# Optimization experiments

Hardware: AMD Instinct MI355X
Metric: run time of the kernel (lower is better)

The kernel has to match this reference:

```python
import jax, jax.numpy as jnp
import numpy as np
from jax import lax

INPUT_SIZE = 512
THRESHOLD = 0.5
IOU_TH = 0.3
MAX_ROIS = 32   # py_cpu_nms(...)[:32]
ROI = 7
NEG = jnp.float32(-1e30)


def _make_anchors(fh, fw, stride):
    # 3 scales x 3 ratios = 9 anchors per cell, laid out in (h, w, anchor)
    # order to match permute(0,2,3,1).view(-1) of the conv heads.
    scales = np.array([32.0, 64.0, 128.0])
    ratios = np.array([0.5, 1.0, 2.0])
    ws = (scales[:, None] * np.sqrt(ratios)[None, :]).reshape(-1)
    hs = (scales[:, None] / np.sqrt(ratios)[None, :]).reshape(-1)
    cy = (np.arange(fh) + 0.5) * stride
    cx = (np.arange(fw) + 0.5) * stride
    CX, CY = np.meshgrid(cx, cy)
    CX = CX[..., None]; CY = CY[..., None]
    a = np.stack([CX - ws / 2, CY - hs / 2, CX + ws / 2, CY + hs / 2], axis=-1)
    return jnp.asarray(a.reshape(-1, 4), jnp.float32)


def setup_inputs() -> dict:
    key = jax.random.key(0)
    k1, k2, k3 = jax.random.split(key, 3)
    B, C, FH, FW, A, stride = 4, 256, 64, 64, 9, 8
    featureMap = jax.random.normal(k1, (B, C, FH, FW), jnp.float32)
    # small init so sigmoid scores spread across threshold and exp(tw) stays sane
    w_cls = jax.random.normal(k2, (A, C, 3, 3), jnp.float32) * 0.05
    w_loc = jax.random.normal(k3, (4 * A, C, 3, 3), jnp.float32) * 0.01
    prior_anchor = _make_anchors(FH, FW, stride)
    return {"featureMap": featureMap, "prior_anchor": prior_anchor,
            "w_cls": w_cls, "w_loc": w_loc, "stride": stride}


def _conv(x, w):
    return lax.conv_general_dilated(x, w, (1, 1), "SAME",
                                    dimension_numbers=("NCHW", "OIHW", "NCHW"))


def _decode(loc, anchors):
    aw = anchors[:, 2] - anchors[:, 0]
    ah = anchors[:, 3] - anchors[:, 1]
    acx = anchors[:, 0] + 0.5 * aw
    acy = anchors[:, 1] + 0.5 * ah
    cx = acx + loc[:, 0] * aw
    cy = acy + loc[:, 1] * ah
    w = aw * jnp.exp(loc[:, 2])
    h = ah * jnp.exp(loc[:, 3])
    return jnp.stack([cx - 0.5 * w, cy - 0.5 * h, cx + 0.5 * w, cy + 0.5 * h], axis=1)


def _iou_one(box, boxes):
    xx1 = jnp.maximum(box[0], boxes[:, 0]); yy1 = jnp.maximum(box[1], boxes[:, 1])
    xx2 = jnp.minimum(box[2], boxes[:, 2]); yy2 = jnp.minimum(box[3], boxes[:, 3])
    inter = jnp.clip(xx2 - xx1, 0) * jnp.clip(yy2 - yy1, 0)
    a1 = (box[2] - box[0]) * (box[3] - box[1])
    a2 = (boxes[:, 2] - boxes[:, 0]) * (boxes[:, 3] - boxes[:, 1])
    return inter / (a1 + a2 - inter + 1e-9)


def _nms(boxes, scores, valid):
    # greedy NMS, fixed MAX_ROIS rounds (== sort-by-score py_cpu_nms + [:32])
    N = scores.shape[0]
    s0 = jnp.where(valid, scores, -1.0)

    def body(i, carry):
        s, picks, ok = carry
        idx = jnp.argmax(s)
        good = s[idx] > 0.0
        picks = picks.at[i].set(idx.astype(jnp.int32))
        ok = ok.at[i].set(good)
        sup = (_iou_one(boxes[idx], boxes) > IOU_TH) | (jnp.arange(N) == idx)
        return (jnp.where(sup, -1.0, s), picks, ok)

    _, picks, ok = lax.fori_loop(
        0, MAX_ROIS, body,
        (s0, jnp.zeros(MAX_ROIS, jnp.int32), jnp.zeros(MAX_ROIS, bool)))
    return picks, ok


def _ceil_div(a, b):
    return -(-a // b)


def _adaptive_maxpool(feat, box):
    # feat: [C, FH, FW]; box: int32 [x1, y1, x2, y2] in feature-map coords.
    # Faithful F.adaptive_max_pool2d bins: start=floor(i*h/7), end=ceil((i+1)*h/7).
    FH, FW = feat.shape[1], feat.shape[2]
    x1, y1, x2, y2 = box[0], box[1], box[2], box[3]
    h = y2 - y1; w = x2 - x1
    i = jnp.arange(ROI)
    rs = y1 + (i * h) // ROI; re = y1 + _ceil_div((i + 1) * h, ROI)
    cs = x1 + (i * w) // ROI; ce = x1 + _ceil_div((i + 1) * w, ROI)
    hh = jnp.arange(FH); ww = jnp.arange(FW)
    rm = jnp.where((hh >= rs[:, None]) & (hh < re[:, None]), 0.0, NEG)  # [7, FH]
    cm = jnp.where((ww >= cs[:, None]) & (ww < ce[:, None]), 0.0, NEG)  # [7, FW]
    t = jnp.max(feat[None] + rm[:, None, :, None], axis=2)              # [7, C, FW]
    out = jnp.max(t[:, None] + cm[None, :, None, :], axis=3)            # [7, 7, C]
    return jnp.transpose(out, (2, 0, 1))                                # [C, 7, 7]


def reference(featureMap, prior_anchor, w_cls, w_loc, stride):
    B, C, FH, FW = featureMap.shape
    cls = jax.nn.sigmoid(_conv(featureMap, w_cls))                      # [B, A, FH, FW]
    cls = jnp.transpose(cls, (0, 2, 3, 1)).reshape(B, -1)               # [B, N]
    loc = jnp.transpose(_conv(featureMap, w_loc), (0, 2, 3, 1)).reshape(B, -1, 4)
    boxes = jax.vmap(_decode, in_axes=(0, None))(loc, prior_anchor)     # [B, N, 4]
    boxes = jnp.clip(boxes, 0.0, float(INPUT_SIZE))                     # clamp(0, input_size)
    valid = (cls > THRESHOLD) \
          & (boxes[..., 2] - boxes[..., 0] >= 2 * stride) \
          & (boxes[..., 3] - boxes[..., 1] >= 2 * stride)
    picks, ok = jax.vmap(_nms)(boxes, cls, valid)                       # [B, 32]
    sel_boxes = jnp.take_along_axis(boxes, picks[..., None], axis=1)    # [B, 32, 4]
    sel_scores = jnp.take_along_axis(cls, picks, axis=1)                # [B, 32]
    eval_boxes = jnp.where(
        ok[..., None],
        jnp.concatenate([sel_boxes, sel_scores[..., None]], axis=-1), 0.0)
    # src_coordinate.int() / stride -> integer feature-map coords
    ib = sel_boxes.astype(jnp.int32) // stride
    fx1 = jnp.clip(ib[..., 0], 0, FW - 1); fy1 = jnp.clip(ib[..., 1], 0, FH - 1)
    fx2 = jnp.clip(ib[..., 2], fx1 + 1, FW); fy2 = jnp.clip(ib[..., 3], fy1 + 1, FH)
    fb = jnp.stack([fx1, fy1, fx2, fy2], axis=-1).reshape(-1, 4)        # [B*32, 4]
    img = jnp.repeat(jnp.arange(B), MAX_ROIS)
    rois = lax.map(lambda a: _adaptive_maxpool(featureMap[a[1]], a[0]), (fb, img))
    rois = jnp.where(ok.reshape(-1)[:, None, None, None], rois, 0.0)    # [B*32, 256, 7, 7]
    return eval_boxes, ok, rois
```

## Files before the change

kernel.cpp:

```cpp
#include <hip/hip_runtime.h>
#include <hip/hip_bf16.h>

#define FHH 64
#define FWW 64
#define CIN 256
#define NB 4
#define NA 9
#define NANCH 36864
#define NPOS 4096
#define OC_TOTAL 45
#define OCP 48
#define MAXROIS 32
#define ROI 7
#define NEGV -1e30f
#define NCHUNK 576
#define NTH 16

typedef unsigned long long u64;

__global__ __launch_bounds__(256) void wtrans_kernel(
    const float* __restrict__ wcls,
    const float* __restrict__ wloc,
    float* __restrict__ wT,
    int* __restrict__ gcnt)
{
    if (blockIdx.x == 0 && threadIdx.x < NB * NTH) gcnt[threadIdx.x] = 0;
    int idx = blockIdx.x * 256 + threadIdx.x;
    int o = idx % 48;
    int rest = idx / 48;
    int tap = rest % 9;
    int c = rest / 9;
    float v = 0.f;
    if (o < OC_TOTAL) {
        v = (o < NA) ? wcls[((size_t)o * CIN + c) * 9 + tap]
                     : wloc[((size_t)(o - NA) * CIN + c) * 9 + tap];
    }
    wT[idx] = v;
}

__global__ __launch_bounds__(256) void conv_kernel(
    const float* __restrict__ feat,
    const float* __restrict__ wT,
    float* __restrict__ partial,
    int nkg, int cpk)
{
    __shared__ float flds[16][18][20];

    int blk = blockIdx.x;
    int low = blk & 7;
    int rest = blk >> 3;
    int kg = rest % nkg;
    int uhi = rest / nkg;
    int unit = uhi * 8 + low;
    int b = unit >> 4;
    int tile = unit & 15;

    int ty0 = (tile >> 2) * 16;
    int tx0 = (tile & 3) * 16;

    int pb = threadIdx.x & 63;
    int q = __builtin_amdgcn_readfirstlane(threadIdx.x >> 6);
    int ry0 = (pb >> 3) * 2;
    int rx0 = (pb & 7) * 2;

    int cbase = kg * cpk;

    float acc[2][2][12];
#pragma unroll
    for (int py = 0; py < 2; ++py)
#pragma unroll
        for (int px = 0; px < 2; ++px)
#pragma unroll
            for (int o = 0; o < 12; ++o) acc[py][px][o] = 0.f;

    for (int c0 = 0; c0 < cpk; c0 += 16) {
        __syncthreads();
        for (int idx = threadIdx.x; idx < 16 * 324; idx += 256) {
            int c = idx / 324;
            int r = idx - c * 324;
            int y = r / 18;
            int x = r - y * 18;
            int gy = ty0 + y - 1;
            int gx = tx0 + x - 1;
            float v = 0.f;
            if ((unsigned)gy < FHH && (unsigned)gx < FWW)
                v = feat[((size_t)(b * CIN + cbase + c0 + c) * FHH + gy) * FWW + gx];
            flds[c][y][x] = v;
        }
        __syncthreads();

        const float* wq = wT + (size_t)(cbase + c0) * 432 + q * 12;
        for (int c = 0; c < 16; ++c) {
            float f[4][4];
#pragma unroll
            for (int r = 0; r < 4; ++r) {
                float2 a0 = *(const float2*)&flds[c][ry0 + r][rx0];
                float2 a1 = *(const float2*)&flds[c][ry0 + r][rx0 + 2];
                f[r][0] = a0.x; f[r][1] = a0.y; f[r][2] = a1.x; f[r][3] = a1.y;
            }
#pragma unroll
            for (int tap = 0; tap < 9; ++tap) {
                int dy = tap / 3, dx = tap % 3;
                const float* wp = wq + (c * 9 + tap) * 48;
                float w[12];
#pragma unroll
                for (int o = 0; o < 12; ++o) w[o] = wp[o];
#pragma unroll
                for (int py = 0; py < 2; ++py)
#pragma unroll
                for (int px = 0; px < 2; ++px) {
                    float fv = f[py + dy][px + dx];
#pragma unroll
                    for (int o = 0; o < 12; ++o)
                        acc[py][px][o] += fv * w[o];
                }
            }
        }
    }

    float* pout = partial + ((size_t)kg * NB + b) * OCP * NPOS;
#pragma unroll
    for (int o = 0; o < 12; ++o) {
        int oo = q * 12 + o;
        float* op = pout + (size_t)oo * NPOS;
#pragma unroll
        for (int py = 0; py < 2; ++py)
#pragma unroll
        for (int px = 0; px < 2; ++px) {
            int pos = (ty0 + ry0 + py) * FWW + (tx0 + rx0 + px);
            op[pos] = acc[py][px][o];
        }
    }
}

__global__ __launch_bounds__(256) void decode_kernel(
    const float* __restrict__ partial,
    const float* __restrict__ anchors,
    const int* __restrict__ stridep,
    float* __restrict__ boxes,
    float* __restrict__ scores,
    int* __restrict__ gcnt,
    int nkg)
{
    const float TH[NTH] = {0.999f, 0.998f, 0.996f, 0.993f, 0.99f, 0.985f,
                           0.98f, 0.975f, 0.97f, 0.965f, 0.96f, 0.95f,
                           0.94f, 0.93f, 0.9f, 0.0f};
    __shared__ int hcnt[NTH];
    if (threadIdx.x < NTH) hcnt[threadIdx.x] = 0;
    __syncthreads();

    int t = blockIdx.x * 256 + threadIdx.x;
    int pos = t & (NPOS - 1);
    int ba = t >> 12;
    int b = ba / 9;
    int a = ba - b * 9;

    float cls = 0.f, l0 = 0.f, l1 = 0.f, l2 = 0.f, l3 = 0.f;
    for (int kg = 0; kg < nkg; ++kg) {
        const float* pk = partial + ((size_t)kg * NB + b) * OCP * NPOS;
        cls += pk[(size_t)a * NPOS + pos];
        l0 += pk[(size_t)(NA + a * 4 + 0) * NPOS + pos];
        l1 += pk[(size_t)(NA + a * 4 + 1) * NPOS + pos];
        l2 += pk[(size_t)(NA + a * 4 + 2) * NPOS + pos];
        l3 += pk[(size_t)(NA + a * 4 + 3) * NPOS + pos];
    }

    float sig = 1.f / (1.f + expf(-cls));
    int n = pos * NA + a;
    const float* an = anchors + (size_t)n * 4;
    float ax1 = an[0], ay1 = an[1], ax2 = an[2], ay2 = an[3];
    float aw = ax2 - ax1, ah = ay2 - ay1;
    float acx = ax1 + 0.5f * aw, acy = ay1 + 0.5f * ah;
    float cx = acx + l0 * aw;
    float cy = acy + l1 * ah;
    float w = aw * expf(l2);
    float h = ah * expf(l3);
    float x1 = fminf(fmaxf(cx - 0.5f * w, 0.f), 512.f);
    float y1 = fminf(fmaxf(cy - 0.5f * h, 0.f), 512.f);
    float x2 = fminf(fmaxf(cx + 0.5f * w, 0.f), 512.f);
    float y2 = fminf(fmaxf(cy + 0.5f * h, 0.f), 512.f);
    int stride = stridep[0];
    float msz = 2.f * (float)stride;
    bool valid = (sig > 0.5f) && ((x2 - x1) >= msz) && ((y2 - y1) >= msz);
    ((float4*)boxes)[(size_t)b * NANCH + n] = make_float4(x1, y1, x2, y2);
    scores[(size_t)b * NANCH + n] = valid ? sig : -1.0f;

#pragma unroll
    for (int i = 0; i < NTH; ++i) {
        u64 mb = __ballot(valid && sig >= TH[i]);
        if ((threadIdx.x & 63) == 0 && mb)
            atomicAdd(&hcnt[i], (int)__popcll(mb));
    }
    __syncthreads();
    if (threadIdx.x < NTH && hcnt[threadIdx.x])
        atomicAdd(&gcnt[b * NTH + threadIdx.x], hcnt[threadIdx.x]);
}

__global__ __launch_bounds__(64) void choose_kernel(
    const int* __restrict__ gcnt,
    float* __restrict__ Tsel, int* __restrict__ Csel, int* __restrict__ Vsel,
    int* __restrict__ force, int* __restrict__ gcount, int cap)
{
    const float TH[NTH] = {0.999f, 0.998f, 0.996f, 0.993f, 0.99f, 0.985f,
                           0.98f, 0.975f, 0.97f, 0.965f, 0.96f, 0.95f,
                           0.94f, 0.93f, 0.9f, 0.0f};
    int b = threadIdx.x;
    if (b >= NB) return;
    int bestc = 0; float bt = TH[0];
    for (int i = 0; i < NTH; ++i) {
        int c = gcnt[b * NTH + i];
        if (c <= cap && c > bestc) { bestc = c; bt = TH[i]; }
    }
    int frc = (gcnt[b * NTH + 0] > cap) ? 1 : 0;
    if (frc) { bestc = cap; bt = TH[0]; }
    Tsel[b] = bt; Csel[b] = bestc; Vsel[b] = gcnt[b * NTH + NTH - 1];
    force[b] = frc; gcount[b] = 0;
}

__global__ __launch_bounds__(256) void nms_compact_kernel(
    const float* __restrict__ scores,
    const float* __restrict__ Tsel,
    int* __restrict__ gcount,
    u64* __restrict__ candkey,
    int cap)
{
    __shared__ int lcnt;
    __shared__ int wbase[4];
    __shared__ int gbase;
    int t = blockIdx.x * 256 + threadIdx.x;
    int b = t / NANCH;
    int j = t - b * NANCH;
    int lane = threadIdx.x & 63;
    int w = threadIdx.x >> 6;
    if (threadIdx.x == 0) lcnt = 0;
    __syncthreads();
    float v = scores[t];
    float T = Tsel[b];
    bool p = (v > 0.f) && (v >= T);
    u64 m = __ballot(p);
    int cnt = (int)__popcll(m);
    if (lane == 0) wbase[w] = atomicAdd(&lcnt, cnt);
    __syncthreads();
    if (threadIdx.x == 0) gbase = lcnt ? atomicAdd(&gcount[b], lcnt) : 0;
    __syncthreads();
    if (p) {
        int off = (int)__popcll(m & ((1ULL << lane) - 1ULL));
        int slot = gbase + wbase[w] + off;
        if (slot < cap)
            candkey[(size_t)b * cap + slot] =
                ((u64)__float_as_uint(v) << 32) | (unsigned int)(~j);
    }
}

__device__ __forceinline__ void write_outputs(
    int b, int i, bool okv, int idx, float sc,
    const float4* Bb4, const int* stridep,
    float* d_out, int* ifb, int* iok)
{
    float4 bb = Bb4[idx];
    float* eb = d_out + ((size_t)b * MAXROIS + i) * 5;
    eb[0] = okv ? bb.x : 0.f;
    eb[1] = okv ? bb.y : 0.f;
    eb[2] = okv ? bb.z : 0.f;
    eb[3] = okv ? bb.w : 0.f;
    eb[4] = okv ? sc : 0.f;
    d_out[NB * MAXROIS * 5 + b * MAXROIS + i] = okv ? 1.f : 0.f;
    int st = stridep[0];
    int fx1 = min(max(((int)bb.x) / st, 0), FWW - 1);
    int fy1 = min(max(((int)bb.y) / st, 0), FHH - 1);
    int fx2 = min(max(((int)bb.z) / st, fx1 + 1), FWW);
    int fy2 = min(max(((int)bb.w) / st, fy1 + 1), FHH);
    int r = b * MAXROIS + i;
    ifb[r * 4 + 0] = fx1;
    ifb[r * 4 + 1] = fy1;
    ifb[r * 4 + 2] = fx2;
    ifb[r * 4 + 3] = fy2;
    iok[r] = okv ? 1 : 0;
}

__global__ __launch_bounds__(1024) void nms_sortscan_kernel(
    const u64* __restrict__ candkey,
    const float* __restrict__ boxes,
    const int* __restrict__ Csel, const int* __restrict__ Vsel,
    const int* __restrict__ force,
    const int* __restrict__ stridep,
    float* __restrict__ d_out,
    int* __restrict__ ifb, int* __restrict__ iok, int* __restrict__ flag,
    int cap)
{
    __shared__ u64 skey[2048];
    __shared__ float4 box_l[2048];
    __shared__ u64 mask[32];
    __shared__ int picks[MAXROIS];
    __shared__ int np_sh;

    int b = blockIdx.x;
    int tid = threadIdx.x;
    int lane = tid & 63;
    int C = Csel[b];
    if (tid == 0) np_sh = 0;

    int CSZ = 64;
    while (CSZ < C) CSZ <<= 1;

    for (int j = tid; j < CSZ; j += 1024)
        skey[j] = (j < C) ? candkey[(size_t)b * cap + j] : 0ULL;

    for (int kk = 2; kk <= CSZ; kk <<= 1) {
        for (int jj = kk >> 1; jj > 0; jj >>= 1) {
            __syncthreads();
            for (int tt = tid; tt < (CSZ >> 1); tt += 1024) {
                int i = ((tt & ~(jj - 1)) << 1) | (tt & (jj - 1));
                int l = i + jj;
                u64 a = skey[i], c2 = skey[l];
                bool up = ((i & kk) == 0);
                bool sw = up ? (a < c2) : (a > c2);
                if (sw) { skey[i] = c2; skey[l] = a; }
            }
        }
    }
    __syncthreads();

    const float4* Bb4 = (const float4*)(boxes + (size_t)b * NANCH * 4);
    for (int j = tid; j < C; j += 1024) {
        int id = (int)(~((unsigned int)(skey[j] & 0xFFFFFFFFULL)));
        box_l[j] = Bb4[id];
    }
    if (tid < 32) {
        int base = tid * 64;
        u64 m0;
        if (base >= C) m0 = ~0ULL;
        else if (base + 64 > C) m0 = ~((1ULL << (C - base)) - 1ULL);
        else m0 = 0ULL;
        mask[tid] = m0;
    }
    __syncthreads();

    for (int round = 0; round < MAXROIS; ++round) {
        u64 mw = (lane < 32) ? mask[lane] : ~0ULL;
        int bpos = __ffsll((u64)(~mw));
        int cand = bpos ? lane * 64 + bpos - 1 : 0x7FFFFFFF;
#pragma unroll
        for (int off = 32; off >= 1; off >>= 1)
            cand = min(cand, __shfl_xor(cand, off));
        int pj = cand;
        if (pj == 0x7FFFFFFF) break;
        if (tid == 0) {
            picks[round] = pj;
            np_sh = round + 1;
            atomicOr(&mask[pj >> 6], 1ULL << (pj & 63));
        }
        float4 pb = box_l[pj];
        float parea = (pb.z - pb.x) * (pb.w - pb.y);
        int j0 = tid * 2;
        u64 curm = mask[tid >> 5];
        u64 addm = 0ULL;
#pragma unroll
        for (int d = 0; d < 2; ++d) {
            int j = j0 + d;
            if (j > pj && j < C && !((curm >> (j & 63)) & 1ULL)) {
                float4 bb2 = box_l[j];
                float xx1 = fmaxf(pb.x, bb2.x), yy1 = fmaxf(pb.y, bb2.y);
                float xx2 = fminf(pb.z, bb2.z), yy2 = fminf(pb.w, bb2.w);
                float inter = fmaxf(xx2 - xx1, 0.f) * fmaxf(yy2 - yy1, 0.f);
                float a2 = (bb2.z - bb2.x) * (bb2.w - bb2.y);
                float iou = inter / (parea + a2 - inter + 1e-9f);
                if (iou > 0.3f) addm |= 1ULL << (j & 63);
            }
        }
        if (addm) atomicOr(&mask[tid >> 5], addm);
        __syncthreads();
    }
    __syncthreads();

    int np = np_sh;
    bool need_fb = force[b] || (np < MAXROIS && Vsel[b] > C);
    if (tid == 0) flag[b] = need_fb ? 1 : 0;
    if (!need_fb && tid < MAXROIS) {
        int i = tid;
        bool okv = i < np;
        int slot = okv ? picks[i] : 0;
        u64 k = skey[slot];
        int idx = okv ? (int)(~((unsigned int)(k & 0xFFFFFFFFULL))) : 0;
        float sc = okv ? __uint_as_float((unsigned int)(k >> 32)) : 0.f;
        write_outputs(b, i, okv, idx, sc, Bb4, stridep, d_out, ifb, iok);
    }
}

__global__ __launch_bounds__(1024) void nms_fallback_kernel(
    const float* __restrict__ boxes,
    const float* __restrict__ scores,
    const int* __restrict__ stridep,
    float* __restrict__ d_out,
    int* __restrict__ ifb,
    int* __restrict__ iok,
    const int* __restrict__ flag)
{
    __shared__ float s[NANCH];
    __shared__ float2 cmax[NCHUNK];
    __shared__ int   picks_sh[MAXROIS];
    __shared__ float pscore_sh[MAXROIS];

    int b = blockIdx.x;
    if (flag[b] == 0) return;

    const float4* Bb4 = (const float4*)(boxes + (size_t)b * NANCH * 4);
    const float* Sb = scores + (size_t)b * NANCH;
    int lane = threadIdx.x & 63;
    int w = threadIdx.x >> 6;

    for (int k = 0; k < 36; ++k) {
        int ch = w * 36 + k;
        int j = ch * 64 + lane;
        float v = Sb[j];
        s[j] = v;
        float bv = v; int bi = j;
#pragma unroll
        for (int off = 32; off >= 1; off >>= 1) {
            float ov = __shfl_xor(bv, off);
            int   oi = __shfl_xor(bi, off);
            if (ov > bv || (ov == bv && oi < bi)) { bv = ov; bi = oi; }
        }
        if (lane == 0) cmax[ch] = make_float2(bv, __int_as_float(bi));
    }
    __syncthreads();
    if (w != 0) return;

    float px1 = 0.f, py1 = 0.f, px2 = 0.f, py2 = 0.f, parea = 0.f;
    int np = 0;
    while (np < MAXROIS) {
        float bv = -2.f; int bi = 0x7fffffff;
#pragma unroll
        for (int k = 0; k < 9; ++k) {
            float2 cm = cmax[lane * 9 + k];
            int ci = __float_as_int(cm.y);
            if (cm.x > bv || (cm.x == bv && ci < bi)) { bv = cm.x; bi = ci; }
        }
#pragma unroll
        for (int off = 32; off >= 1; off >>= 1) {
            float ov = __shfl_xor(bv, off);
            int   oi = __shfl_xor(bi, off);
            if (ov > bv || (ov == bv && oi < bi)) { bv = ov; bi = oi; }
        }
        if (bv <= 0.f) break;
        int fi = bi; float fs = bv;

        float4 cbb = Bb4[fi];

        bool sup = false;
        if (lane < np) {
            float xx1 = fmaxf(px1, cbb.x), yy1 = fmaxf(py1, cbb.y);
            float xx2 = fminf(px2, cbb.z), yy2 = fminf(py2, cbb.w);
            float inter = fmaxf(xx2 - xx1, 0.f) * fmaxf(yy2 - yy1, 0.f);
            float a2 = (cbb.z - cbb.x) * (cbb.w - cbb.y);
            float iou = inter / (parea + a2 - inter + 1e-9f);
            sup = iou > 0.3f;
        }
        u64 m = __ballot(sup);

        int ch = fi >> 6;
        int j = ch * 64 + lane;
        float sv = (j == fi) ? -1.f : s[j];
        if (j == fi) s[j] = -1.f;
        float nv = sv; int ni = j;
#pragma unroll
        for (int off = 32; off >= 1; off >>= 1) {
            float ov = __shfl_xor(nv, off);
            int   oi = __shfl_xor(ni, off);
            if (ov > nv || (ov == nv && oi < ni)) { nv = ov; ni = oi; }
        }
        if (lane == 0) cmax[ch] = make_float2(nv, __int_as_float(ni));

        if (m == 0ULL) {
            if (lane == np) {
                px1 = cbb.x; py1 = cbb.y; px2 = cbb.z; py2 = cbb.w;
                parea = (px2 - px1) * (py2 - py1);
            }
            picks_sh[np] = fi;
            pscore_sh[np] = fs;
            ++np;
        }
    }

    if (lane < MAXROIS) {
        int i = lane;
        bool okv = i < np;
        int idx = okv ? picks_sh[i] : 0;
        float sc = okv ? pscore_sh[i] : 0.f;
        write_outputs(b, i, okv, idx, sc, Bb4, stridep, d_out, ifb, iok);
    }
}

__global__ __launch_bounds__(256) void roi_kernel(
    const float* __restrict__ feat,
    const int* __restrict__ ifb,
    const int* __restrict__ iok,
    float* __restrict__ out_rois)
{
    int t = blockIdx.x * 256 + threadIdx.x;
    int bin = t % 49;
    int rc = t / 49;
    int c = rc & 255;
    int r = rc >> 8;
    int i = bin / 7;
    int j = bin - i * 7;

    if (!iok[r]) { out_rois[t] = 0.f; return; }

    int x1 = ifb[r * 4 + 0];
    int y1 = ifb[r * 4 + 1];
    int x2 = ifb[r * 4 + 2];
    int y2 = ifb[r * 4 + 3];
    int h = y2 - y1;
    int w = x2 - x1;
    int b = r >> 5;

    int rs = y1 + (i * h) / ROI;
    int re = y1 + ((i + 1) * h + ROI - 1) / ROI;
    int cs = x1 + (j * w) / ROI;
    int ce = x1 + ((j + 1) * w + ROI - 1) / ROI;

    const float* F = feat + (size_t)(b * CIN + c) * NPOS;
    float m = NEGV;
    for (int y = rs; y < re; ++y) {
        const float* row = F + y * FWW;
        for (int x = cs; x < ce; ++x) m = fmaxf(m, row[x]);
    }
    out_rois[t] = m;
}

extern "C" void kernel_launch(void* const* d_in, const int* in_sizes, int n_in,
                              void* d_out, int out_size, void* d_ws, size_t ws_size,
                              hipStream_t stream) {
    const float* feat    = (const float*)d_in[0];
    const float* anchors = (const float*)d_in[1];
    const float* wcls    = (const float*)d_in[2];
    const float* wloc    = (const float*)d_in[3];
    const int*   stridep = (const int*)d_in[4];
    float* out = (float*)d_out;
    float* ws  = (float*)d_ws;

    const size_t P1 = (size_t)NB * OCP * NPOS;
    const size_t WTN = 256 * 9 * 48;

    auto need = [&](int nk, int cp) -> size_t {
        size_t f = P1 * nk
                 + 589824 + 147456 + WTN
                 + (size_t)NB * cp * 2
                 + 2048;
        return f * 4;
    };
    int nkg = 16, cap = 2048;
    if (ws_size < need(16, 2048)) {
        if (ws_size >= need(8, 2048)) { nkg = 8; }
        else if (ws_size >= need(4, 2048)) { nkg = 4; }
        else { nkg = 4; cap = 1024; }
    }

    float* partial   = ws;
    float* boxes     = partial + P1 * nkg;
    float* scores    = boxes + (size_t)NB * NANCH * 4;
    float* wT        = scores + (size_t)NB * NANCH;
    u64*   candkey   = (u64*)(wT + WTN);
    float* tailf     = (float*)(candkey + (size_t)NB * cap);
    int*   ifb       = (int*)tailf;
    int*   iok       = ifb + 512;
    int*   flag      = iok + 128;
    int*   gcnt      = flag + 4;
    float* Tsel      = (float*)(gcnt + 64);
    int*   Csel      = (int*)(Tsel + 4);
    int*   Vsel      = Csel + 4;
    int*   force     = Vsel + 4;
    int*   gcount    = force + 4;

    wtrans_kernel<<<432, 256, 0, stream>>>(wcls, wloc, wT, gcnt);
    conv_kernel<<<64 * nkg, 256, 0, stream>>>(feat, wT, partial, nkg, CIN / nkg);
    decode_kernel<<<(NB * NANCH) / 256, 256, 0, stream>>>(partial, anchors, stridep, boxes, scores, gcnt, nkg);
    choose_kernel<<<1, 64, 0, stream>>>(gcnt, Tsel, Csel, Vsel, force, gcount, cap);
    nms_compact_kernel<<<(NB * NANCH) / 256, 256, 0, stream>>>(scores, Tsel, gcount, candkey, cap);
    nms_sortscan_kernel<<<NB, 1024, 0, stream>>>(candkey, boxes, Csel, Vsel, force, stridep, out, ifb, iok, flag, cap);
    nms_fallback_kernel<<<NB, 1024, 0, stream>>>(boxes, scores, stridep, out, ifb, iok, flag);
    roi_kernel<<<(NB * MAXROIS * CIN * 49) / 256, 256, 0, stream>>>(feat, ifb, iok, out + NB * MAXROIS * 5 + NB * MAXROIS);
}
```

Baseline: 155.9 us.

## Shrink NMS candidate cap, refine threshold ladder, and skip intra-wave bitonic syncs

Fixes the NMS candidate cap at 1024 instead of 2048 and sizes the shared buffers and the sort kernel's thread count (512) to match. Replaces the score threshold ladder with finer, higher steps held in constant memory, so the chosen threshold keeps the candidate set closer to the cap. The bitonic sort now skips `__syncthreads` for stages with compare distance below 128, which stay inside one 64-lane wavefront. This relies on lockstep execution and LDS visibility within a wavefront. The smaller cap also raises the chance that the fallback path is forced.

```diff
diff --git a/kernel.cpp b/kernel.cpp
--- a/kernel.cpp
+++ b/kernel.cpp
@@ -15,8 +15,13 @@
 #define NEGV -1e30f
 #define NCHUNK 576
 #define NTH 16
+#define CAP 1024
 
 typedef unsigned long long u64;
+
+__device__ __constant__ const float TH_LADDER[NTH] = {
+    0.9999f, 0.9998f, 0.9995f, 0.999f, 0.998f, 0.997f, 0.995f, 0.993f,
+    0.99f, 0.987f, 0.984f, 0.98f, 0.975f, 0.97f, 0.96f, 0.0f};
 
 __global__ __launch_bounds__(256) void wtrans_kernel(
     const float* __restrict__ wcls,
@@ -142,9 +147,6 @@
     int* __restrict__ gcnt,
     int nkg)
 {
-    const float TH[NTH] = {0.999f, 0.998f, 0.996f, 0.993f, 0.99f, 0.985f,
-                           0.98f, 0.975f, 0.97f, 0.965f, 0.96f, 0.95f,
-                           0.94f, 0.93f, 0.9f, 0.0f};
     __shared__ int hcnt[NTH];
     if (threadIdx.x < NTH) hcnt[threadIdx.x] = 0;
     __syncthreads();
@@ -187,7 +189,7 @@
 
 #pragma unroll
     for (int i = 0; i < NTH; ++i) {
-        u64 mb = __ballot(valid && sig >= TH[i]);
+        u64 mb = __ballot(valid && sig >= TH_LADDER[i]);
         if ((threadIdx.x & 63) == 0 && mb)
             atomicAdd(&hcnt[i], (int)__popcll(mb));
     }
@@ -201,18 +203,15 @@
     float* __restrict__ Tsel, int* __restrict__ Csel, int* __restrict__ Vsel,
     int* __restrict__ force, int* __restrict__ gcount, int cap)
 {
-    const float TH[NTH] = {0.999f, 0.998f, 0.996f, 0.993f, 0.99f, 0.985f,
-                           0.98f, 0.975f, 0.97f, 0.965f, 0.96f, 0.95f,
-                           0.94f, 0.93f, 0.9f, 0.0f};
     int b = threadIdx.x;
     if (b >= NB) return;
-    int bestc = 0; float bt = TH[0];
+    int bestc = 0; float bt = TH_LADDER[0];
     for (int i = 0; i < NTH; ++i) {
         int c = gcnt[b * NTH + i];
-        if (c <= cap && c > bestc) { bestc = c; bt = TH[i]; }
+        if (c <= cap && c > bestc) { bestc = c; bt = TH_LADDER[i]; }
     }
     int frc = (gcnt[b * NTH + 0] > cap) ? 1 : 0;
-    if (frc) { bestc = cap; bt = TH[0]; }
+    if (frc) { bestc = cap; bt = TH_LADDER[0]; }
     Tsel[b] = bt; Csel[b] = bestc; Vsel[b] = gcnt[b * NTH + NTH - 1];
     force[b] = frc; gcount[b] = 0;
 }
@@ -278,7 +277,7 @@
     iok[r] = okv ? 1 : 0;
 }
 
-__global__ __launch_bounds__(1024) void nms_sortscan_kernel(
+__global__ __launch_bounds__(512) void nms_sortscan_kernel(
     const u64* __restrict__ candkey,
     const float* __restrict__ boxes,
     const int* __restrict__ Csel, const int* __restrict__ Vsel,
@@ -288,9 +287,9 @@
     int* __restrict__ ifb, int* __restrict__ iok, int* __restrict__ flag,
     int cap)
 {
-    __shared__ u64 skey[2048];
-    __shared__ float4 box_l[2048];
-    __shared__ u64 mask[32];
+    __shared__ u64 skey[CAP];
+    __shared__ float4 box_l[CAP];
+    __shared__ u64 mask[CAP / 64];
     __shared__ int picks[MAXROIS];
     __shared__ int np_sh;
 
@@ -303,13 +302,15 @@
     int CSZ = 64;
     while (CSZ < C) CSZ <<= 1;
 
-    for (int j = tid; j < CSZ; j += 1024)
+    for (int j = tid; j < CSZ; j += 512)
         skey[j] = (j < C) ? candkey[(size_t)b * cap + j] : 0ULL;
 
+    int prev_cross = 1;
     for (int kk = 2; kk <= CSZ; kk <<= 1) {
         for (int jj = kk >> 1; jj > 0; jj >>= 1) {
-            __syncthreads();
-            for (int tt = tid; tt < (CSZ >> 1); tt += 1024) {
+            int cross = (jj >= 128) ? 1 : 0;
+            if (cross || prev_cross) __syncthreads();
+            for (int tt = tid; tt < (CSZ >> 1); tt += 512) {
                 int i = ((tt & ~(jj - 1)) << 1) | (tt & (jj - 1));
                 int l = i + jj;
                 u64 a = skey[i], c2 = skey[l];
@@ -317,16 +318,17 @@
                 bool sw = up ? (a < c2) : (a > c2);
                 if (sw) { skey[i] = c2; skey[l] = a; }
             }
+            prev_cross = cross;
         }
     }
     __syncthreads();
 
     const float4* Bb4 = (const float4*)(boxes + (size_t)b * NANCH * 4);
-    for (int j = tid; j < C; j += 1024) {
+    for (int j = tid; j < C; j += 512) {
         int id = (int)(~((unsigned int)(skey[j] & 0xFFFFFFFFULL)));
         box_l[j] = Bb4[id];
     }
-    if (tid < 32) {
+    if (tid < CAP / 64) {
         int base = tid * 64;
         u64 m0;
         if (base >= C) m0 = ~0ULL;
@@ -337,7 +339,7 @@
     __syncthreads();
 
     for (int round = 0; round < MAXROIS; ++round) {
-        u64 mw = (lane < 32) ? mask[lane] : ~0ULL;
+        u64 mw = (lane < CAP / 64) ? mask[lane] : ~0ULL;
         int bpos = __ffsll((u64)(~mw));
         int cand = bpos ? lane * 64 + bpos - 1 : 0x7FFFFFFF;
 #pragma unroll
@@ -542,19 +544,19 @@
 
     const size_t P1 = (size_t)NB * OCP * NPOS;
     const size_t WTN = 256 * 9 * 48;
-
-    auto need = [&](int nk, int cp) -> size_t {
+    const int cap = CAP;
+
+    auto need = [&](int nk) -> size_t {
         size_t f = P1 * nk
                  + 589824 + 147456 + WTN
-                 + (size_t)NB * cp * 2
+                 + (size_t)NB * cap * 2
                  + 2048;
         return f * 4;
     };
-    int nkg = 16, cap = 2048;
-    if (ws_size < need(16, 2048)) {
-        if (ws_size >= need(8, 2048)) { nkg = 8; }
-        else if (ws_size >= need(4, 2048)) { nkg = 4; }
-        else { nkg = 4; cap = 1024; }
+    int nkg = 16;
+    if (ws_size < need(16)) {
+        if (ws_size >= need(8)) { nkg = 8; }
+        else { nkg = 4; }
     }
 
     float* partial   = ws;
@@ -578,7 +580,7 @@
     decode_kernel<<<(NB * NANCH) / 256, 256, 0, stream>>>(partial, anchors, stridep, boxes, scores, gcnt, nkg);
     choose_kernel<<<1, 64, 0, stream>>>(gcnt, Tsel, Csel, Vsel, force, gcount, cap);
     nms_compact_kernel<<<(NB * NANCH) / 256, 256, 0, stream>>>(scores, Tsel, gcount, candkey, cap);
-    nms_sortscan_kernel<<<NB, 1024, 0, stream>>>(candkey, boxes, Csel, Vsel, force, stridep, out, ifb, iok, flag, cap);
+    nms_sortscan_kernel<<<NB, 512, 0, stream>>>(candkey, boxes, Csel, Vsel, force, stridep, out, ifb, iok, flag, cap);
     nms_fallback_kernel<<<NB, 1024, 0, stream>>>(boxes, scores, stridep, out, ifb, iok, flag);
     roi_kernel<<<(NB * MAXROIS * CIN * 49) / 256, 256, 0, stream>>>(feat, ifb, iok, out + NB * MAXROIS * 5 + NB * MAXROIS);
 }
```

New measurement: 140.1 us. 1.11x faster.
